# Optimization experiments

Hardware: AMD Instinct MI355X
Metric: run time of the kernel (lower is better)

Reference implementation:

```python
import jax, jax.numpy as jnp
import numpy as np

DIM, HEADS, KV_HEADS = 1024, 16, 4
B, T = 1, 4096
HEAD_DIM = DIM // HEADS           # 64
KV_DIM = DIM // (HEADS // KV_HEADS)  # 256
SCALE = HEAD_DIM ** -0.5


def setup_inputs() -> dict:
    key = jax.random.key(0)
    ks = jax.random.split(key, 9)
    s = lambda fan_in: fan_in ** -0.5
    return {
        "x": jax.random.normal(ks[0], (B, T, DIM), jnp.float32),
        "mask": jnp.tril(jnp.ones((1, 1, T, T), jnp.bool_)),  # causal
        "q_w": jax.random.normal(ks[1], (DIM, DIM), jnp.float32) * s(DIM),
        "q_b": jnp.zeros((DIM,), jnp.float32),
        "k_w": jax.random.normal(ks[2], (KV_DIM, DIM), jnp.float32) * s(DIM),
        "k_b": jnp.zeros((KV_DIM,), jnp.float32),
        "v_w": jax.random.normal(ks[3], (KV_DIM, DIM), jnp.float32) * s(DIM),
        "v_b": jnp.zeros((KV_DIM,), jnp.float32),
        "o_w": jax.random.normal(ks[4], (DIM, DIM), jnp.float32) * s(DIM),
        "o_b": jnp.zeros((DIM,), jnp.float32),
    }


def reference(x, mask, q_w, q_b, k_w, k_b, v_w, v_b, o_w, o_b):
    b, t, d = x.shape
    g = HEADS // KV_HEADS  # query heads per kv head
    # projections (torch Linear: x @ W^T + b)
    q = (x @ q_w.T + q_b).reshape(b, t, HEADS, HEAD_DIM).transpose(0, 2, 1, 3)      # [B,H,T,hd]
    k = (x @ k_w.T + k_b).reshape(b, t, KV_HEADS, HEAD_DIM).transpose(0, 2, 1, 3)   # [B,Hk,T,hd]
    v = (x @ v_w.T + v_b).reshape(b, t, KV_HEADS, HEAD_DIM).transpose(0, 2, 1, 3)   # [B,Hk,T,hd]
    # GQA: group query heads over shared kv heads
    qg = q.reshape(b, KV_HEADS, g, t, HEAD_DIM)                                     # [B,Hk,g,T,hd]
    scores = jnp.einsum('bkgtd,bksd->bkgts', qg, k) * SCALE                         # [B,Hk,g,T,T]
    scores = jnp.where(mask[:, :, None, :, :], scores, -1e9)
    attn = jax.nn.softmax(scores, axis=-1)  # dropout is identity in eval mode
    out = jnp.einsum('bkgts,bksd->bkgtd', attn, v)                                  # [B,Hk,g,T,hd]
    out = out.reshape(b, HEADS, t, HEAD_DIM).transpose(0, 2, 1, 3).reshape(b, t, d)
    out = out @ o_w.T + o_b
    return out, k, v  # (output, new kv cache)
```

## Files before the change

### kernel.cpp

```cpp
#include <hip/hip_runtime.h>
#include <hip/hip_bf16.h>
#include <stdint.h>

typedef __bf16 bf16;
typedef __bf16 bf16x8 __attribute__((ext_vector_type(8)));
typedef float  f32x4 __attribute__((ext_vector_type(4)));

#define SEQ   4096
#define DIM_  1024
#define HD_   64
#define NEG_BIG (-30000.0f)

__device__ __forceinline__ bf16x8 cvt8(const float* p) {
    f32x4 a = *(const f32x4*)p, b = *(const f32x4*)(p + 4);
    bf16x8 r;
    r[0]=(bf16)a[0]; r[1]=(bf16)a[1]; r[2]=(bf16)a[2]; r[3]=(bf16)a[3];
    r[4]=(bf16)b[0]; r[5]=(bf16)b[1]; r[6]=(bf16)b[2]; r[7]=(bf16)b[3];
    return r;
}

__global__ __launch_bounds__(256)
void cvt_pre(const float* __restrict__ x,
             const float* __restrict__ qw, const float* __restrict__ kw,
             const float* __restrict__ vw,
             const float* __restrict__ qb, const float* __restrict__ kb,
             const float* __restrict__ vb,
             bf16* __restrict__ x_bf, bf16* __restrict__ wcat,
             float* __restrict__ bcat)
{
    const int NX = (SEQ * DIM_) / 8;
    const int NW = (1536 * 1024) / 8;
    int i = blockIdx.x * 256 + threadIdx.x;
    if (i < NX) {
        *(bf16x8*)(x_bf + (size_t)i * 8) = cvt8(x + (size_t)i * 8);
    } else if (i < NX + NW) {
        int e = (i - NX) * 8;
        const float* src;
        if (e < 1024 * 1024)      src = qw + e;
        else if (e < 1280 * 1024) src = kw + (e - 1024 * 1024);
        else                      src = vw + (e - 1280 * 1024);
        *(bf16x8*)(wcat + e) = cvt8(src);
    }
    if (i < 1536)
        bcat[i] = (i < 1024) ? qb[i] : (i < 1280) ? kb[i - 1024] : vb[i - 1280];
}

template<int MODE>
__global__ __launch_bounds__(256)
void gemm_bt(const bf16* __restrict__ A, const void* __restrict__ Bw,
             const float* __restrict__ bias_all,
             float* __restrict__ C0, float* __restrict__ C1, float* __restrict__ C2,
             bf16* __restrict__ Qbf, bf16* __restrict__ Kbf, bf16* __restrict__ VTbf)
{
    const int K = 1024;
    const int tid  = threadIdx.x;
    const int lane = tid & 63, wave = tid >> 6;
    const int qd = lane >> 4, ln = lane & 15;
    const int wm = (wave & 1) * 64, wn = (wave >> 1) * 64;
    const int m0 = blockIdx.x * 128, n0 = blockIdx.y * 128;

    const bf16*  Bpb = (MODE == 1) ? (const bf16*)Bw + (size_t)n0 * K : nullptr;
    const float* Bpf = (MODE == 0) ? (const float*)Bw + (size_t)n0 * K : nullptr;
    const float* bias = bias_all + n0;

    __shared__ bf16 As[128*32];
    __shared__ bf16 Bs[128*32];

    f32x4 acc[4][4] = {};

    for (int k0 = 0; k0 < K; k0 += 32) {
        bf16x8 ra[2], rb[2];
        #pragma unroll
        for (int i = 0; i < 2; ++i) {
            int s   = i*256 + tid;
            int row = s >> 2, ch = s & 3;
            ra[i] = *(const bf16x8*)(A + (size_t)(m0+row)*K + k0 + ch*8);
            if (MODE == 1)
                rb[i] = *(const bf16x8*)(Bpb + (size_t)row*K + k0 + ch*8);
            else
                rb[i] = cvt8(Bpf + (size_t)row*K + k0 + ch*8);
        }
        __syncthreads();
        #pragma unroll
        for (int i = 0; i < 2; ++i) {
            int s   = i*256 + tid;
            int row = s >> 2, ch = s & 3;
            *(bf16x8*)(As + row*32 + ch*8) = ra[i];
            *(bf16x8*)(Bs + row*32 + ch*8) = rb[i];
        }
        __syncthreads();

        bf16x8 af[4], bg[4];
        #pragma unroll
        for (int i = 0; i < 4; ++i)
            af[i] = *(const bf16x8*)(As + (wm + i*16 + ln)*32 + qd*8);
        #pragma unroll
        for (int j = 0; j < 4; ++j)
            bg[j] = *(const bf16x8*)(Bs + (wn + j*16 + ln)*32 + qd*8);

        #pragma unroll
        for (int i = 0; i < 4; ++i)
            #pragma unroll
            for (int j = 0; j < 4; ++j)
                acc[i][j] = __builtin_amdgcn_mfma_f32_16x16x32_bf16(af[i], bg[j], acc[i][j], 0, 0, 0);
    }

    #pragma unroll
    for (int i = 0; i < 4; ++i) {
        #pragma unroll
        for (int j = 0; j < 4; ++j) {
            int colg = n0 + wn + j*16 + ln;
            float bv = bias[wn + j*16 + ln];
            #pragma unroll
            for (int r = 0; r < 4; ++r) {
                int rowg = m0 + wm + i*16 + qd*4 + r;
                float v = acc[i][j][r] + bv;
                if (MODE == 0) {
                    C0[(size_t)rowg*1024 + colg] = v;
                } else if (colg < 1024) {
                    Qbf[(size_t)rowg*1024 + colg] = (bf16)(v * 0.125f);
                } else if (colg < 1280) {
                    int c2 = colg - 1024;
                    size_t idx = (size_t)(c2 >> 6)*(SEQ*HD_) + (size_t)rowg*HD_ + (c2 & 63);
                    C1[idx]  = v;
                    Kbf[idx] = (bf16)v;
                } else {
                    int c2 = colg - 1280;
                    C2[(size_t)(c2 >> 6)*(SEQ*HD_) + (size_t)rowg*HD_ + (c2 & 63)] = v;
                    VTbf[(size_t)(c2 >> 6)*(HD_*SEQ) + (size_t)(c2 & 63)*SEQ + rowg] = (bf16)v;
                }
            }
        }
    }
}

__global__ __launch_bounds__(256)
void attn_fwd(const bf16* __restrict__ Q, const bf16* __restrict__ Kc,
              const bf16* __restrict__ VT, bf16* __restrict__ att)
{
    const int bid  = blockIdx.x;
    const int head = bid & 15;
    const int mt   = 63 - (bid >> 4);
    const int qb   = mt * 64;
    const int kvh  = head >> 2;

    const int tid = threadIdx.x, lane = tid & 63, wave = tid >> 6;
    const int qd = lane >> 4, ln = lane & 15;
    const int rw0 = qb + wave * 16;

    __shared__ bf16 Ks[64*72];
    __shared__ bf16 Vt[64*72];
    __shared__ bf16 Ps[4][16*72];

    const bf16* Kbase = Kc + (size_t)kvh * SEQ * HD_;
    const bf16* Vbase = VT + (size_t)kvh * HD_ * SEQ;

    bf16x8 aq[2];
    #pragma unroll
    for (int ks = 0; ks < 2; ++ks)
        aq[ks] = *(const bf16x8*)(Q + (size_t)(rw0 + ln)*DIM_ + head*HD_ + ks*32 + qd*8);

    f32x4 o[4] = {};
    float l_p[4] = {0.f, 0.f, 0.f, 0.f};

    const float LOG2E = 1.4426950408889634f;
    const float C16   = 16.0f * LOG2E;
    const int nkt = mt + 1;

    for (int kt = 0; kt < nkt; ++kt) {
        const int kb = kt * 64;

        bf16x8 rk[2], rv[2];
        #pragma unroll
        for (int i = 0; i < 2; ++i) {
            int s = i*256 + tid;
            int r8 = s >> 3, ch = s & 7;
            rk[i] = *(const bf16x8*)(Kbase + (size_t)(kb + r8)*HD_ + ch*8);
            rv[i] = *(const bf16x8*)(Vbase + (size_t)r8*SEQ + kb + ch*8);
        }
        __syncthreads();
        #pragma unroll
        for (int i = 0; i < 2; ++i) {
            int s = i*256 + tid;
            int r8 = s >> 3, ch = s & 7;
            *(bf16x8*)(Ks + r8*72 + ch*8) = rk[i];
            *(bf16x8*)(Vt + r8*72 + ch*8) = rv[i];
        }
        __syncthreads();

        f32x4 S[4] = {};
        #pragma unroll
        for (int ks = 0; ks < 2; ++ks) {
            bf16x8 bk[4];
            #pragma unroll
            for (int nf = 0; nf < 4; ++nf)
                bk[nf] = *(const bf16x8*)(Ks + (nf*16 + ln)*72 + ks*32 + qd*8);
            #pragma unroll
            for (int nf = 0; nf < 4; ++nf)
                S[nf] = __builtin_amdgcn_mfma_f32_16x16x32_bf16(aq[ks], bk[nf], S[nf], 0, 0, 0);
        }

        if (kt == nkt - 1) {
            #pragma unroll
            for (int nf = 0; nf < 4; ++nf) {
                int col = kb + nf*16 + ln;
                #pragma unroll
                for (int r = 0; r < 4; ++r) {
                    int row = rw0 + qd*4 + r;
                    if (col > row) S[nf][r] = NEG_BIG;
                }
            }
        }

        bf16* Pw = &Ps[wave][0];
        #pragma unroll
        for (int r = 0; r < 4; ++r) {
            #pragma unroll
            for (int nf = 0; nf < 4; ++nf) {
                float p = exp2f(S[nf][r] * LOG2E - C16);
                l_p[r] += p;
                Pw[(qd*4 + r)*72 + nf*16 + ln] = (bf16)p;
            }
        }
        asm volatile("s_waitcnt lgkmcnt(0)" ::: "memory");

        #pragma unroll
        for (int ks = 0; ks < 2; ++ks) {
            bf16x8 bv[4];
            #pragma unroll
            for (int nf = 0; nf < 4; ++nf)
                bv[nf] = *(const bf16x8*)(Vt + (nf*16 + ln)*72 + ks*32 + qd*8);
            bf16x8 ap = *(const bf16x8*)(&Ps[wave][ln*72 + ks*32 + qd*8]);
            #pragma unroll
            for (int nf = 0; nf < 4; ++nf)
                o[nf] = __builtin_amdgcn_mfma_f32_16x16x32_bf16(ap, bv[nf], o[nf], 0, 0, 0);
        }
    }

    #pragma unroll
    for (int r = 0; r < 4; ++r) {
        float l = l_p[r];
        l += __shfl_xor(l, 1);
        l += __shfl_xor(l, 2);
        l += __shfl_xor(l, 4);
        l += __shfl_xor(l, 8);
        float inv = 1.0f / l;
        int trow = rw0 + qd*4 + r;
        #pragma unroll
        for (int nf = 0; nf < 4; ++nf)
            att[(size_t)trow*DIM_ + head*HD_ + nf*16 + ln] = (bf16)(o[nf][r] * inv);
    }
}

extern "C" void kernel_launch(void* const* d_in, const int* in_sizes, int n_in,
                              void* d_out, int out_size, void* d_ws, size_t ws_size,
                              hipStream_t stream)
{
    const float* x  = (const float*)d_in[0];
    const float* qw = (const float*)d_in[2];
    const float* qb = (const float*)d_in[3];
    const float* kw = (const float*)d_in[4];
    const float* kb = (const float*)d_in[5];
    const float* vw = (const float*)d_in[6];
    const float* vb = (const float*)d_in[7];
    const float* ow = (const float*)d_in[8];
    const float* ob = (const float*)d_in[9];

    float* out  = (float*)d_out;
    float* kout = out  + (size_t)SEQ * DIM_;
    float* vout = kout + (size_t)4 * SEQ * HD_;

    bf16*  q_bf  = (bf16*)d_out;
    bf16*  k_bf  = q_bf + (size_t)SEQ * DIM_;
    bf16*  vT_bf = k_bf + (size_t)4 * SEQ * HD_;
    bf16*  wcat  = vT_bf + (size_t)4 * HD_ * SEQ;
    float* bcat  = (float*)(wcat + (size_t)1536*1024);
    bf16* x_bf = (bf16*)d_ws;
    bf16* att  = (bf16*)d_ws;

    cvt_pre<<<dim3(2816), 256, 0, stream>>>(x, qw, kw, vw, qb, kb, vb,
                                            x_bf, wcat, bcat);
    gemm_bt<1><<<dim3(32, 12), 256, 0, stream>>>(x_bf, wcat, bcat,
                                                 nullptr, kout, vout,
                                                 q_bf, k_bf, vT_bf);
    attn_fwd<<<dim3(1024), 256, 0, stream>>>(q_bf, k_bf, vT_bf, att);
    gemm_bt<0><<<dim3(32, 8), 256, 0, stream>>>(att, ow, ob,
                                                out, nullptr, nullptr,
                                                nullptr, nullptr, nullptr);
}
```

Baseline: 274.3 us.

## Use direct global-to-LDS loads in GEMM and move K/V bf16 conversion to separate kernel

The GEMM tile loads now go straight from global memory into LDS through global_load_lds, replacing the register round trip. Each iteration is followed by a full waitcnt. The scattered bf16 K and transposed-V stores are removed from the projection GEMM epilogue. A new kv_cvt kernel reads the fp32 K/V cache back, converts it, and transposes V through shared memory with coalesced writes. This trades strided uncoalesced epilogue stores for an extra launch and an extra read of K/V, and the unpadded LDS layout may cause bank conflicts.

```diff
diff --git a/kernel.cpp b/kernel.cpp
--- a/kernel.cpp
+++ b/kernel.cpp
@@ -17,6 +17,12 @@
     r[0]=(bf16)a[0]; r[1]=(bf16)a[1]; r[2]=(bf16)a[2]; r[3]=(bf16)a[3];
     r[4]=(bf16)b[0]; r[5]=(bf16)b[1]; r[6]=(bf16)b[2]; r[7]=(bf16)b[3];
     return r;
+}
+
+__device__ __forceinline__ void async_cp16(const bf16* g, bf16* l) {
+    __builtin_amdgcn_global_load_lds(
+        (const __attribute__((address_space(1))) void*)g,
+        (__attribute__((address_space(3))) void*)l, 16, 0, 0);
 }
 
 __global__ __launch_bounds__(256)
@@ -45,12 +51,46 @@
         bcat[i] = (i < 1024) ? qb[i] : (i < 1280) ? kb[i - 1024] : vb[i - 1280];
 }
 
+__global__ __launch_bounds__(256)
+void kv_cvt(const float* __restrict__ kout, const float* __restrict__ vout,
+            bf16* __restrict__ k_bf, bf16* __restrict__ vT_bf)
+{
+    const int b   = blockIdx.x;
+    const int kvh = b >> 6, tb = b & 63;
+    const int tid = threadIdx.x;
+
+    __shared__ bf16 T[64*72];
+
+    const float* Ksrc = kout + ((size_t)kvh*SEQ + tb*64) * HD_;
+    const float* Vsrc = vout + ((size_t)kvh*SEQ + tb*64) * HD_;
+
+    #pragma unroll
+    for (int i = 0; i < 2; ++i) {
+        int s = i*256 + tid;
+        int r = s >> 3, c = s & 7;
+        bf16x8 k8 = cvt8(Ksrc + (size_t)r*HD_ + c*8);
+        *(bf16x8*)(k_bf + ((size_t)kvh*SEQ + tb*64 + r)*HD_ + c*8) = k8;
+        bf16x8 v8 = cvt8(Vsrc + (size_t)r*HD_ + c*8);
+        #pragma unroll
+        for (int e = 0; e < 8; ++e)
+            T[(c*8 + e)*72 + r] = v8[e];
+    }
+    __syncthreads();
+    #pragma unroll
+    for (int i = 0; i < 2; ++i) {
+        int s = i*256 + tid;
+        int d = s >> 3, c = s & 7;
+        *(bf16x8*)(vT_bf + ((size_t)kvh*HD_ + d)*SEQ + tb*64 + c*8) =
+            *(const bf16x8*)(T + d*72 + c*8);
+    }
+}
+
 template<int MODE>
 __global__ __launch_bounds__(256)
 void gemm_bt(const bf16* __restrict__ A, const void* __restrict__ Bw,
              const float* __restrict__ bias_all,
              float* __restrict__ C0, float* __restrict__ C1, float* __restrict__ C2,
-             bf16* __restrict__ Qbf, bf16* __restrict__ Kbf, bf16* __restrict__ VTbf)
+             bf16* __restrict__ Qbf)
 {
     const int K = 1024;
     const int tid  = threadIdx.x;
@@ -69,25 +109,27 @@
     f32x4 acc[4][4] = {};
 
     for (int k0 = 0; k0 < K; k0 += 32) {
-        bf16x8 ra[2], rb[2];
+        bf16x8 rb[2];
+        if (MODE == 0) {
+            #pragma unroll
+            for (int i = 0; i < 2; ++i) {
+                int s = i*256 + tid;
+                int row = s >> 2, ch = s & 3;
+                rb[i] = cvt8(Bpf + (size_t)row*K + k0 + ch*8);
+            }
+        }
+        __syncthreads();
         #pragma unroll
         for (int i = 0; i < 2; ++i) {
             int s   = i*256 + tid;
             int row = s >> 2, ch = s & 3;
-            ra[i] = *(const bf16x8*)(A + (size_t)(m0+row)*K + k0 + ch*8);
+            async_cp16(A + (size_t)(m0+row)*K + k0 + ch*8, As + s*8);
             if (MODE == 1)
-                rb[i] = *(const bf16x8*)(Bpb + (size_t)row*K + k0 + ch*8);
+                async_cp16(Bpb + (size_t)row*K + k0 + ch*8, Bs + s*8);
             else
-                rb[i] = cvt8(Bpf + (size_t)row*K + k0 + ch*8);
-        }
-        __syncthreads();
-        #pragma unroll
-        for (int i = 0; i < 2; ++i) {
-            int s   = i*256 + tid;
-            int row = s >> 2, ch = s & 3;
-            *(bf16x8*)(As + row*32 + ch*8) = ra[i];
-            *(bf16x8*)(Bs + row*32 + ch*8) = rb[i];
-        }
+                *(bf16x8*)(Bs + s*8) = rb[i];
+        }
+        __builtin_amdgcn_s_waitcnt(0);
         __syncthreads();
 
         bf16x8 af[4], bg[4];
@@ -121,13 +163,10 @@
                     Qbf[(size_t)rowg*1024 + colg] = (bf16)(v * 0.125f);
                 } else if (colg < 1280) {
                     int c2 = colg - 1024;
-                    size_t idx = (size_t)(c2 >> 6)*(SEQ*HD_) + (size_t)rowg*HD_ + (c2 & 63);
-                    C1[idx]  = v;
-                    Kbf[idx] = (bf16)v;
+                    C1[(size_t)(c2 >> 6)*(SEQ*HD_) + (size_t)rowg*HD_ + (c2 & 63)] = v;
                 } else {
                     int c2 = colg - 1280;
                     C2[(size_t)(c2 >> 6)*(SEQ*HD_) + (size_t)rowg*HD_ + (c2 & 63)] = v;
-                    VTbf[(size_t)(c2 >> 6)*(HD_*SEQ) + (size_t)(c2 & 63)*SEQ + rowg] = (bf16)v;
                 }
             }
         }
@@ -281,10 +320,9 @@
     cvt_pre<<<dim3(2816), 256, 0, stream>>>(x, qw, kw, vw, qb, kb, vb,
                                             x_bf, wcat, bcat);
     gemm_bt<1><<<dim3(32, 12), 256, 0, stream>>>(x_bf, wcat, bcat,
-                                                 nullptr, kout, vout,
-                                                 q_bf, k_bf, vT_bf);
+                                                 nullptr, kout, vout, q_bf);
+    kv_cvt<<<dim3(256), 256, 0, stream>>>(kout, vout, k_bf, vT_bf);
     attn_fwd<<<dim3(1024), 256, 0, stream>>>(q_bf, k_bf, vT_bf, att);
     gemm_bt<0><<<dim3(32, 8), 256, 0, stream>>>(att, ow, ob,
-                                                out, nullptr, nullptr,
-                                                nullptr, nullptr, nullptr);
-}
+                                                out, nullptr, nullptr, nullptr);
+}
```

After: 271.8 us. Within noise of the previous version (-0.9%).
